# Kernel optimization log

Measured on AMD Instinct MI355X. Metric: run time of the kernel, lower is better.

Reference implementation:

```python
import jax, jax.numpy as jnp
import numpy as np

B, S, E, H = 2, 2048, 1024, 16
DH = E // H  # 64


def setup_inputs() -> dict:
    key = jax.random.key(0)
    ks = jax.random.split(key, 5)
    scale = 1.0 / np.sqrt(E)
    x = jax.random.normal(ks[0], (B, S, E), dtype=jnp.float32)
    # stacked per-head kqv Linear weights: out = x @ Wkqv[h] + bkqv[h], producing (k, q, v) chunks
    Wkqv = jax.random.normal(ks[1], (H, E, 3 * DH), dtype=jnp.float32) * scale
    bkqv = jax.random.normal(ks[2], (H, 3 * DH), dtype=jnp.float32) * scale
    Wo = jax.random.normal(ks[3], (E, E), dtype=jnp.float32) * scale
    bo = jax.random.normal(ks[4], (E,), dtype=jnp.float32) * scale
    return {"x": x, "Wkqv": Wkqv, "bkqv": bkqv, "Wo": Wo, "bo": bo}


def reference(x, Wkqv, bkqv, Wo, bo):
    b, s, e = x.shape
    h, _, f = Wkqv.shape
    dh = f // 3
    # per-head projection, fused over heads: [b, h, s, 3*dh]
    kqv = jnp.einsum('bse,hef->bhsf', x, Wkqv) + bkqv[None, :, None, :]
    # chunk order in the original is k, q, v
    k, q, v = jnp.split(kqv, 3, axis=-1)
    scores = jnp.einsum('bhqd,bhkd->bhqk', q, k) / jnp.sqrt(jnp.asarray(dh, x.dtype))
    causal = jnp.tril(jnp.ones((s, s), dtype=bool))  # slice of the tril buffer
    scores = jnp.where(causal[None, None], scores, -jnp.inf)
    weights = jax.nn.softmax(scores, axis=-1)
    sa = jnp.einsum('bhqk,bhkd->bhqd', weights, v)
    # concat heads along feature dim (head order preserved)
    sa = sa.transpose(0, 2, 1, 3).reshape(b, s, h * dh)
    return sa @ Wo + bo
```

## Files before the change

### kernel.cpp

```cpp
#include <hip/hip_runtime.h>
#include <hip/hip_bf16.h>

typedef __attribute__((ext_vector_type(8))) short bf16x8;
typedef __attribute__((ext_vector_type(4))) float f32x4;
typedef unsigned short u16;

#define NEG_INF (-__builtin_inff())

__device__ __forceinline__ void gload16(const void* g, void* l) {
  __builtin_amdgcn_global_load_lds(
      (const __attribute__((address_space(1))) void*)g,
      (__attribute__((address_space(3))) void*)l, 16, 0, 0);
}

__device__ __forceinline__ u16 f2b(float f) {
  union { float f; unsigned u; } v;
  v.f = f;
  unsigned r = v.u + 0x7fff + ((v.u >> 16) & 1);
  return (u16)(r >> 16);
}

__global__ __launch_bounds__(256) void prep_kernel(
    const float* __restrict__ x, u16* __restrict__ xb,
    const float* __restrict__ Wkqv, u16* __restrict__ WkqvT,
    const float* __restrict__ Wo, u16* __restrict__ WoT) {
  __shared__ u16 t[32][33];
  const int bid = blockIdx.x;
  const int tid = threadIdx.x;
  if (bid < 4096) {
    const int i = bid * 256 + tid;
    float4 v = ((const float4*)x)[i];
    ushort2 a = {f2b(v.x), f2b(v.y)}, b = {f2b(v.z), f2b(v.w)};
    ((ushort2*)xb)[i * 2] = a;
    ((ushort2*)xb)[i * 2 + 1] = b;
    return;
  }
  const int tx = tid & 31, ty = tid >> 5;
  const float* src;
  u16* dst;
  int R, C, bx_, by;
  if (bid < 7168) {
    const int tt = bid - 4096;
    const int bz = tt / 192, rem = tt % 192;
    by = rem / 6; bx_ = rem % 6; R = 1024; C = 192;
    src = Wkqv + (size_t)bz * R * C;
    dst = WkqvT + (size_t)bz * R * C;
  } else {
    const int tt = bid - 7168;
    by = tt >> 5; bx_ = tt & 31; R = 1024; C = 1024;
    src = Wo; dst = WoT;
  }
  const int c0 = bx_ * 32, r0 = by * 32;
  for (int i = ty; i < 32; i += 8)
    t[i][tx] = f2b(src[(size_t)(r0 + i) * C + c0 + tx]);
  __syncthreads();
  for (int i = ty; i < 32; i += 8)
    dst[(size_t)(c0 + i) * R + r0 + tx] = t[tx][i];
}

__device__ __forceinline__ void gemm_mainloop_128(
    const __hip_bfloat16* __restrict__ A, const __hip_bfloat16* __restrict__ Bt,
    int K, int m0, int n0, f32x4 acc[4][4], char* AsB, char* BsB) {
  const int tid = threadIdx.x;
  const int wave = tid >> 6, lane = tid & 63;
  const int lhi = lane >> 4, llo = lane & 15;
  const int wr = wave >> 1, wc = wave & 1;
  f32x4 z = {0.f, 0.f, 0.f, 0.f};
#pragma unroll
  for (int i = 0; i < 4; i++)
#pragma unroll
    for (int j = 0; j < 4; j++) acc[i][j] = z;

#define GSTAGE(c, kk)                                                          \
  {                                                                            \
    char* AsW = AsB + (c)*8192;                                                \
    char* BsW = BsB + (c)*8192;                                                \
    _Pragma("unroll") for (int i = 0; i < 2; i++) {                            \
      int cb = i * 256 + wave * 64;                                            \
      int cq = cb + lane;                                                      \
      gload16(A + ((size_t)(m0 + (cq >> 2)) * K + (kk) + (cq & 3) * 8),        \
              AsW + cb * 16);                                                  \
      gload16(Bt + ((size_t)(n0 + (cq >> 2)) * K + (kk) + (cq & 3) * 8),       \
              BsW + cb * 16);                                                  \
    }                                                                          \
  }

  GSTAGE(0, 0);
  int cur = 0;
  const int nk = K >> 5;
  for (int t = 0; t < nk; t++) {
    if (t + 1 < nk) {
      GSTAGE(cur ^ 1, (t + 1) * 32);
      asm volatile("s_waitcnt vmcnt(4)" ::: "memory");
    } else {
      asm volatile("s_waitcnt vmcnt(0)" ::: "memory");
    }
    __builtin_amdgcn_s_barrier();
    __builtin_amdgcn_sched_barrier(0);

    const char* Ar = AsB + cur * 8192;
    const char* Br = BsB + cur * 8192;
    bf16x8 a[4], b[4];
#pragma unroll
    for (int m4 = 0; m4 < 4; m4++)
      a[m4] = *(const bf16x8*)(Ar + (wr * 64 + m4 * 16 + llo) * 64 + lhi * 16);
#pragma unroll
    for (int n4 = 0; n4 < 4; n4++)
      b[n4] = *(const bf16x8*)(Br + (wc * 64 + n4 * 16 + llo) * 64 + lhi * 16);
#pragma unroll
    for (int m4 = 0; m4 < 4; m4++)
#pragma unroll
      for (int n4 = 0; n4 < 4; n4++)
        acc[m4][n4] =
            __builtin_amdgcn_mfma_f32_16x16x32_bf16(a[m4], b[n4], acc[m4][n4], 0, 0, 0);
    __builtin_amdgcn_sched_barrier(0);
    __builtin_amdgcn_s_barrier();
    cur ^= 1;
  }
#undef GSTAGE
}

__device__ __forceinline__ void gemm_mainloop_64x128(
    const __hip_bfloat16* __restrict__ A, const __hip_bfloat16* __restrict__ Bt,
    int K, int m0, int n0, f32x4 acc[2][4], char* AsB, char* BsB) {
  const int tid = threadIdx.x;
  const int wave = tid >> 6, lane = tid & 63;
  const int lhi = lane >> 4, llo = lane & 15;
  const int wr = wave >> 1, wc = wave & 1;
  f32x4 z = {0.f, 0.f, 0.f, 0.f};
#pragma unroll
  for (int i = 0; i < 2; i++)
#pragma unroll
    for (int j = 0; j < 4; j++) acc[i][j] = z;

#define GSTAGE64(c, kk)                                                        \
  {                                                                            \
    char* AsW = AsB + (c)*4096;                                                \
    char* BsW = BsB + (c)*8192;                                                \
    gload16(A + ((size_t)(m0 + (tid >> 2)) * K + (kk) + (tid & 3) * 8),        \
            AsW + (wave * 64) * 16);                                           \
    _Pragma("unroll") for (int i = 0; i < 2; i++) {                            \
      int cb = i * 256 + wave * 64;                                            \
      int cq = cb + lane;                                                      \
      gload16(Bt + ((size_t)(n0 + (cq >> 2)) * K + (kk) + (cq & 3) * 8),       \
              BsW + cb * 16);                                                  \
    }                                                                          \
  }

  GSTAGE64(0, 0);
  int cur = 0;
  const int nk = K >> 5;
  for (int t = 0; t < nk; t++) {
    if (t + 1 < nk) {
      GSTAGE64(cur ^ 1, (t + 1) * 32);
      asm volatile("s_waitcnt vmcnt(3)" ::: "memory");
    } else {
      asm volatile("s_waitcnt vmcnt(0)" ::: "memory");
    }
    __builtin_amdgcn_s_barrier();
    __builtin_amdgcn_sched_barrier(0);

    const char* Ar = AsB + cur * 4096;
    const char* Br = BsB + cur * 8192;
    bf16x8 a[2], b[4];
#pragma unroll
    for (int m2 = 0; m2 < 2; m2++)
      a[m2] = *(const bf16x8*)(Ar + (wr * 32 + m2 * 16 + llo) * 64 + lhi * 16);
#pragma unroll
    for (int n4 = 0; n4 < 4; n4++)
      b[n4] = *(const bf16x8*)(Br + (wc * 64 + n4 * 16 + llo) * 64 + lhi * 16);
#pragma unroll
    for (int m2 = 0; m2 < 2; m2++)
#pragma unroll
      for (int n4 = 0; n4 < 4; n4++)
        acc[m2][n4] =
            __builtin_amdgcn_mfma_f32_16x16x32_bf16(a[m2], b[n4], acc[m2][n4], 0, 0, 0);
    __builtin_amdgcn_sched_barrier(0);
    __builtin_amdgcn_s_barrier();
    cur ^= 1;
  }
#undef GSTAGE64
}

__global__ __launch_bounds__(256) void kqv_gemm(
    const __hip_bfloat16* __restrict__ x, const __hip_bfloat16* __restrict__ WT,
    const float* __restrict__ bkqv, __hip_bfloat16* __restrict__ Qb,
    __hip_bfloat16* __restrict__ Kb, __hip_bfloat16* __restrict__ Vt) {
  __shared__ __align__(16) char As[16384];
  __shared__ __align__(16) char Bs[16384];
  const int m0 = blockIdx.y * 128, n0 = blockIdx.x * 128;
  f32x4 acc[4][4];
  gemm_mainloop_128(x, WT, 1024, m0, n0, acc, As, Bs);

  const int tid = threadIdx.x, wave = tid >> 6, lane = tid & 63;
  const int lhi = lane >> 4, llo = lane & 15;
  const int wr = wave >> 1, wc = wave & 1;
#pragma unroll
  for (int m4 = 0; m4 < 4; m4++)
#pragma unroll
    for (int n4 = 0; n4 < 4; n4++)
#pragma unroll
      for (int r = 0; r < 4; r++) {
        int mg = m0 + wr * 64 + m4 * 16 + lhi * 4 + r;
        int ng = n0 + wc * 64 + n4 * 16 + llo;
        int b = mg >> 11, s = mg & 2047;
        int h = ng / 192, f = ng % 192;
        float v = acc[m4][n4][r] + bkqv[h * 192 + f];
        int chunk = f >> 6, d = f & 63;
        size_t bh = (size_t)(b * 16 + h);
        if (chunk == 0)
          Kb[(bh * 2048 + s) * 64 + d] = __float2bfloat16(v);
        else if (chunk == 1)
          Qb[(bh * 2048 + s) * 64 + d] = __float2bfloat16(v * 0.180336880f);
        else
          Vt[(bh * 64 + d) * 2048 + s] = __float2bfloat16(v);
      }
}

__global__ __launch_bounds__(256) void attn_kernel(
    const __hip_bfloat16* __restrict__ Qb, const __hip_bfloat16* __restrict__ Kb,
    const __hip_bfloat16* __restrict__ Vt, __hip_bfloat16* __restrict__ SA) {
  __shared__ __align__(16) char lds[40960];
  const int orig = blockIdx.x;
  const int bh = (orig & 7) * 4 + ((orig >> 3) & 3);
  const int qt = 31 - (orig >> 5);
  const int nt = qt + 1;
  const int b = bh >> 4, h = bh & 15;
  const int tid = threadIdx.x, wave = tid >> 6, lane = tid & 63;
  const int lhi = lane >> 4, llo = lane & 15;
  const int lhi4 = lhi * 4;

  const __hip_bfloat16* qp =
      Qb + ((size_t)bh * 2048 + qt * 64 + wave * 16 + llo) * 64 + lhi * 8;
  bf16x8 q0 = *(const bf16x8*)qp, q1 = *(const bf16x8*)(qp + 32);

  const char* Kg = (const char*)(Kb + (size_t)bh * 2048 * 64);
  const char* Vg = (const char*)(Vt + (size_t)bh * 64 * 2048);
  char* PsB = lds + 32768 + wave * 2048;

  f32x4 z = {0.f, 0.f, 0.f, 0.f};
  f32x4 o[4];
  float m_s = NEG_INF, l_s = 0.f;
#pragma unroll
  for (int i = 0; i < 4; i++) o[i] = z;
  const int qg = qt * 64 + wave * 16 + llo;
  const int qg0 = qt * 64 + wave * 16 + lhi4;

#define STAGE(c, k0)                                                          \
  {                                                                           \
    char* KsW = lds + (c)*8192;                                               \
    char* VsW = lds + 16384 + (c)*8192;                                       \
    _Pragma("unroll") for (int i = 0; i < 2; i++) {                           \
      int ch = i * 256 + tid;                                                 \
      int soff = (ch * 16) ^ (((ch >> 3) & 7) << 4);                          \
      gload16(Kg + (size_t)(k0)*128 + soff, KsW + (i * 256 + wave * 64) * 16);\
      int dd = ch >> 3, c8 = ch & 7;                                          \
      int boff = (c8 * 16) ^ ((dd & 7) << 4);                                 \
      gload16(Vg + (size_t)dd * 4096 + (size_t)(k0)*2 + boff,                 \
              VsW + (i * 256 + wave * 64) * 16);                              \
    }                                                                         \
  }

  STAGE(0, 0);
  int cur = 0;

  for (int T = 0; T < nt; T++) {
    if (T + 1 < nt) {
      STAGE(cur ^ 1, (T + 1) * 64);
      asm volatile("s_waitcnt vmcnt(4)" ::: "memory");
    } else {
      asm volatile("s_waitcnt vmcnt(0)" ::: "memory");
    }
    __builtin_amdgcn_s_barrier();
    __builtin_amdgcn_sched_barrier(0);

    const int k0 = T * 64;
    const bool masked = (T == nt - 1);
    const char* KsB = lds + cur * 8192;
    const char* VsB = lds + 16384 + cur * 8192;

    f32x4 s[4] = {z, z, z, z};
#pragma unroll
    for (int j = 0; j < 4; j++) {
      const int row = j * 16 + llo;
      const int rx = (row & 7) << 4;
      bf16x8 bk0 = *(const bf16x8*)(KsB + ((row * 128 + lhi * 16) ^ rx));
      bf16x8 bk1 = *(const bf16x8*)(KsB + ((row * 128 + 64 + lhi * 16) ^ rx));
      s[j] = __builtin_amdgcn_mfma_f32_16x16x32_bf16(bk0, q0, s[j], 0, 0, 0);
      s[j] = __builtin_amdgcn_mfma_f32_16x16x32_bf16(bk1, q1, s[j], 0, 0, 0);
    }

    if (masked) {
#pragma unroll
      for (int j = 0; j < 4; j++)
#pragma unroll
        for (int r = 0; r < 4; r++)
          if (k0 + j * 16 + lhi4 + r > qg) s[j][r] = NEG_INF;
    }
    float pmax = s[0][0];
#pragma unroll
    for (int j = 0; j < 4; j++)
#pragma unroll
      for (int r = 0; r < 4; r++) pmax = fmaxf(pmax, s[j][r]);
    pmax = fmaxf(pmax, __shfl_xor(pmax, 16));
    pmax = fmaxf(pmax, __shfl_xor(pmax, 32));
    if (!__all(pmax - m_s <= 5.0f)) {
      const float mn = fmaxf(m_s, pmax);
      const float sc = __builtin_exp2f(m_s - mn);
      m_s = mn;
      l_s *= sc;
#pragma unroll
      for (int r = 0; r < 4; r++) {
        const float scr = __shfl(sc, lhi4 + r);
#pragma unroll
        for (int n4 = 0; n4 < 4; n4++) o[n4][r] *= scr;
      }
    }
    const int px = (llo & 7) << 4;
    float ps = 0.f;
#pragma unroll
    for (int j = 0; j < 4; j++) {
      ushort4 pw;
#pragma unroll
      for (int r = 0; r < 4; r++) {
        const float p = __builtin_exp2f(s[j][r] - m_s);
        ps += p;
        ((__hip_bfloat16*)&pw)[r] = __float2bfloat16(p);
      }
      *(ushort4*)(PsB + ((llo * 128 + j * 32 + lhi * 8) ^ px)) = pw;
    }
    l_s += ps;

    {
      bf16x8 ap0 = *(const bf16x8*)(PsB + ((llo * 128 + lhi * 16) ^ px));
      bf16x8 ap1 = *(const bf16x8*)(PsB + ((llo * 128 + 64 + lhi * 16) ^ px));
#pragma unroll
      for (int n4 = 0; n4 < 4; n4++) {
        const int d = n4 * 16 + llo;
        const int dx = (d & 7) << 4;
        bf16x8 bv0 = *(const bf16x8*)(VsB + ((d * 128 + lhi * 16) ^ dx));
        bf16x8 bv1 = *(const bf16x8*)(VsB + ((d * 128 + 64 + lhi * 16) ^ dx));
        o[n4] = __builtin_amdgcn_mfma_f32_16x16x32_bf16(ap0, bv0, o[n4], 0, 0, 0);
        o[n4] = __builtin_amdgcn_mfma_f32_16x16x32_bf16(ap1, bv1, o[n4], 0, 0, 0);
      }
    }
    __builtin_amdgcn_sched_barrier(0);
    __builtin_amdgcn_s_barrier();
    cur ^= 1;
  }

  {
    float l = l_s;
    l += __shfl_xor(l, 16);
    l += __shfl_xor(l, 32);
    const float inv = 1.f / l;
#pragma unroll
    for (int r = 0; r < 4; r++) {
      const float invr = __shfl(inv, lhi4 + r);
      const size_t ob = ((size_t)b * 2048 + qg0 + r) * 1024 + h * 64;
#pragma unroll
      for (int n4 = 0; n4 < 4; n4++)
        SA[ob + n4 * 16 + llo] = __float2bfloat16(o[n4][r] * invr);
    }
  }
#undef STAGE
}

__global__ __launch_bounds__(256) void out_gemm(
    const __hip_bfloat16* __restrict__ SA, const __hip_bfloat16* __restrict__ WoT,
    const float* __restrict__ bo, float* __restrict__ out) {
  __shared__ __align__(16) char As[8192];
  __shared__ __align__(16) char Bs[16384];
  const int m0 = blockIdx.y * 64, n0 = blockIdx.x * 128;
  f32x4 acc[2][4];
  gemm_mainloop_64x128(SA, WoT, 1024, m0, n0, acc, As, Bs);

  const int tid = threadIdx.x, wave = tid >> 6, lane = tid & 63;
  const int lhi = lane >> 4, llo = lane & 15;
  const int wr = wave >> 1, wc = wave & 1;
#pragma unroll
  for (int m2 = 0; m2 < 2; m2++)
#pragma unroll
    for (int n4 = 0; n4 < 4; n4++)
#pragma unroll
      for (int r = 0; r < 4; r++) {
        int mg = m0 + wr * 32 + m2 * 16 + lhi * 4 + r;
        int ng = n0 + wc * 64 + n4 * 16 + llo;
        out[(size_t)mg * 1024 + ng] = acc[m2][n4][r] + bo[ng];
      }
}

extern "C" void kernel_launch(void* const* d_in, const int* in_sizes, int n_in,
                              void* d_out, int out_size, void* d_ws, size_t ws_size,
                              hipStream_t stream) {
  const float* x = (const float*)d_in[0];
  const float* Wkqv = (const float*)d_in[1];
  const float* bkqv = (const float*)d_in[2];
  const float* Wo = (const float*)d_in[3];
  const float* bo = (const float*)d_in[4];
  float* out = (float*)d_out;

  char* w = (char*)d_ws;
  __hip_bfloat16* WkqvT = (__hip_bfloat16*)(w);
  __hip_bfloat16* WoT = (__hip_bfloat16*)(w + 6291456);
  __hip_bfloat16* Qb = (__hip_bfloat16*)(w + 8388608);
  __hip_bfloat16* Kb = (__hip_bfloat16*)(w + 16777216);
  __hip_bfloat16* Vt = (__hip_bfloat16*)(w + 25165824);
  __hip_bfloat16* SAb = (__hip_bfloat16*)(w + 33554432);
  __hip_bfloat16* xb = (__hip_bfloat16*)(w + 41943040);

  prep_kernel<<<8192, 256, 0, stream>>>(x, (u16*)xb, Wkqv, (u16*)WkqvT,
                                        Wo, (u16*)WoT);
  kqv_gemm<<<dim3(24, 32), 256, 0, stream>>>(xb, WkqvT, bkqv, Qb, Kb, Vt);
  attn_kernel<<<1024, 256, 0, stream>>>(Qb, Kb, Vt, SAb);
  out_gemm<<<dim3(8, 64), 256, 0, stream>>>(SAb, WoT, bo, out);
}
```

Measured before the change: 117.2 us.

## Keep attention probabilities in registers via permlane swaps instead of LDS round-trip

```diff
diff --git a/kernel.cpp b/kernel.cpp
--- a/kernel.cpp
+++ b/kernel.cpp
@@ -3,6 +3,8 @@
 
 typedef __attribute__((ext_vector_type(8))) short bf16x8;
 typedef __attribute__((ext_vector_type(4))) float f32x4;
+typedef __attribute__((ext_vector_type(2))) unsigned u32x2;
+typedef __attribute__((ext_vector_type(4))) unsigned u32x4;
 typedef unsigned short u16;
 
 #define NEG_INF (-__builtin_inff())
@@ -18,6 +20,12 @@
   v.f = f;
   unsigned r = v.u + 0x7fff + ((v.u >> 16) & 1);
   return (u16)(r >> 16);
+}
+
+__device__ __forceinline__ unsigned cvt_pk_bf16(float a, float b) {
+  unsigned r;
+  asm("v_cvt_pk_bf16_f32 %0, %1, %2" : "=v"(r) : "v"(a), "v"(b));
+  return r;
 }
 
 __global__ __launch_bounds__(256) void prep_kernel(
@@ -220,7 +228,7 @@
 __global__ __launch_bounds__(256) void attn_kernel(
     const __hip_bfloat16* __restrict__ Qb, const __hip_bfloat16* __restrict__ Kb,
     const __hip_bfloat16* __restrict__ Vt, __hip_bfloat16* __restrict__ SA) {
-  __shared__ __align__(16) char lds[40960];
+  __shared__ __align__(16) char lds[32768];
   const int orig = blockIdx.x;
   const int bh = (orig & 7) * 4 + ((orig >> 3) & 3);
   const int qt = 31 - (orig >> 5);
@@ -236,7 +244,6 @@
 
   const char* Kg = (const char*)(Kb + (size_t)bh * 2048 * 64);
   const char* Vg = (const char*)(Vt + (size_t)bh * 64 * 2048);
-  char* PsB = lds + 32768 + wave * 2048;
 
   f32x4 z = {0.f, 0.f, 0.f, 0.f};
   f32x4 o[4];
@@ -302,8 +309,16 @@
     for (int j = 0; j < 4; j++)
 #pragma unroll
       for (int r = 0; r < 4; r++) pmax = fmaxf(pmax, s[j][r]);
-    pmax = fmaxf(pmax, __shfl_xor(pmax, 16));
-    pmax = fmaxf(pmax, __shfl_xor(pmax, 32));
+    {
+      union { float f; unsigned u; } pu;
+      pu.f = pmax;
+      u32x2 sp = __builtin_amdgcn_permlane32_swap(pu.u, pu.u, false, false);
+      float m1 = fmaxf(__uint_as_float(sp.x), __uint_as_float(sp.y));
+      union { float f; unsigned u; } mu;
+      mu.f = m1;
+      u32x2 tp = __builtin_amdgcn_permlane16_swap(mu.u, mu.u, false, false);
+      pmax = fmaxf(__uint_as_float(tp.x), __uint_as_float(tp.y));
+    }
     if (!__all(pmax - m_s <= 5.0f)) {
       const float mn = fmaxf(m_s, pmax);
       const float sc = __builtin_exp2f(m_s - mn);
@@ -316,33 +331,47 @@
         for (int n4 = 0; n4 < 4; n4++) o[n4][r] *= scr;
       }
     }
-    const int px = (llo & 7) << 4;
+
+    unsigned pk[4][2];
     float ps = 0.f;
 #pragma unroll
     for (int j = 0; j < 4; j++) {
-      ushort4 pw;
-#pragma unroll
-      for (int r = 0; r < 4; r++) {
-        const float p = __builtin_exp2f(s[j][r] - m_s);
-        ps += p;
-        ((__hip_bfloat16*)&pw)[r] = __float2bfloat16(p);
-      }
-      *(ushort4*)(PsB + ((llo * 128 + j * 32 + lhi * 8) ^ px)) = pw;
+      float p0 = __builtin_exp2f(s[j][0] - m_s);
+      float p1 = __builtin_exp2f(s[j][1] - m_s);
+      float p2 = __builtin_exp2f(s[j][2] - m_s);
+      float p3 = __builtin_exp2f(s[j][3] - m_s);
+      ps += (p0 + p1) + (p2 + p3);
+      pk[j][0] = cvt_pk_bf16(p0, p1);
+      pk[j][1] = cvt_pk_bf16(p2, p3);
     }
     l_s += ps;
 
-    {
-      bf16x8 ap0 = *(const bf16x8*)(PsB + ((llo * 128 + lhi * 16) ^ px));
-      bf16x8 ap1 = *(const bf16x8*)(PsB + ((llo * 128 + 64 + lhi * 16) ^ px));
-#pragma unroll
-      for (int n4 = 0; n4 < 4; n4++) {
-        const int d = n4 * 16 + llo;
-        const int dx = (d & 7) << 4;
-        bf16x8 bv0 = *(const bf16x8*)(VsB + ((d * 128 + lhi * 16) ^ dx));
-        bf16x8 bv1 = *(const bf16x8*)(VsB + ((d * 128 + 64 + lhi * 16) ^ dx));
-        o[n4] = __builtin_amdgcn_mfma_f32_16x16x32_bf16(ap0, bv0, o[n4], 0, 0, 0);
-        o[n4] = __builtin_amdgcn_mfma_f32_16x16x32_bf16(ap1, bv1, o[n4], 0, 0, 0);
-      }
+    u32x4 a0w, a1w;
+#pragma unroll
+    for (int u = 0; u < 2; u++) {
+      u32x2 sp = __builtin_amdgcn_permlane32_swap(pk[0][u], pk[1][u], false, false);
+      u32x2 tp = __builtin_amdgcn_permlane16_swap(sp.x, sp.y, false, false);
+      a0w[u] = tp.x;
+      a0w[u + 2] = tp.y;
+    }
+#pragma unroll
+    for (int u = 0; u < 2; u++) {
+      u32x2 sp = __builtin_amdgcn_permlane32_swap(pk[2][u], pk[3][u], false, false);
+      u32x2 tp = __builtin_amdgcn_permlane16_swap(sp.x, sp.y, false, false);
+      a1w[u] = tp.x;
+      a1w[u + 2] = tp.y;
+    }
+    bf16x8 ap0 = __builtin_bit_cast(bf16x8, a0w);
+    bf16x8 ap1 = __builtin_bit_cast(bf16x8, a1w);
+
+#pragma unroll
+    for (int n4 = 0; n4 < 4; n4++) {
+      const int d = n4 * 16 + llo;
+      const int dx = (d & 7) << 4;
+      bf16x8 bv0 = *(const bf16x8*)(VsB + ((d * 128 + lhi * 16) ^ dx));
+      bf16x8 bv1 = *(const bf16x8*)(VsB + ((d * 128 + 64 + lhi * 16) ^ dx));
+      o[n4] = __builtin_amdgcn_mfma_f32_16x16x32_bf16(ap0, bv0, o[n4], 0, 0, 0);
+      o[n4] = __builtin_amdgcn_mfma_f32_16x16x32_bf16(ap1, bv1, o[n4], 0, 0, 0);
     }
     __builtin_amdgcn_sched_barrier(0);
     __builtin_amdgcn_s_barrier();
@@ -350,9 +379,14 @@
   }
 
   {
-    float l = l_s;
-    l += __shfl_xor(l, 16);
-    l += __shfl_xor(l, 32);
+    union { float f; unsigned u; } lu;
+    lu.f = l_s;
+    u32x2 sp = __builtin_amdgcn_permlane32_swap(lu.u, lu.u, false, false);
+    float l1 = __uint_as_float(sp.x) + __uint_as_float(sp.y);
+    union { float f; unsigned u; } l2u;
+    l2u.f = l1;
+    u32x2 tp = __builtin_amdgcn_permlane16_swap(l2u.u, l2u.u, false, false);
+    const float l = __uint_as_float(tp.x) + __uint_as_float(tp.y);
     const float inv = 1.f / l;
 #pragma unroll
     for (int r = 0; r < 4; r++) {
```

Measured after the change: 118.0 us. About the same (+0.7%).
